# Kernel tuning notes

Hardware: AMD Instinct MI355X
Metric: run time of the kernel (lower is better)

Reference implementation:

```python
import jax, jax.numpy as jnp
from jax import lax
import numpy as np

CHANNELS = 16
THRESH = 0.1
UPDATE_RATE = 0.25


def _sobel_kernel():
    ident = np.array([[0., 0., 0.], [0., 1., 0.], [0., 0., 0.]], np.float32)
    sx = np.array([[-1., 0., 1.], [-2., 0., 2.], [-1., 0., 1.]], np.float32)
    sy = sx.T
    k = np.stack([ident, sx, sy])[:, None, :, :]          # [3,1,3,3]
    k = np.tile(k, (CHANNELS, 1, 1, 1))                   # [48,1,3,3] (torch repeat order)
    return jnp.asarray(k)


def _perceive(x, w_sobel):
    # circular pad then depthwise grouped conv (groups=CHANNELS, 3 filters per group)
    xp = jnp.pad(x, ((0, 0), (0, 0), (1, 1), (1, 1)), mode='wrap')
    return lax.conv_general_dilated(
        xp, w_sobel, window_strides=(1, 1), padding='VALID',
        dimension_numbers=('NCHW', 'OIHW', 'NCHW'),
        feature_group_count=CHANNELS)                     # [B,48,H,W]


def _alive_mask(x):
    alpha = x[:, 3:4]                                     # [B,1,H,W]
    p = jnp.pad(alpha, ((0, 0), (0, 0), (1, 1), (1, 1)), mode='wrap')
    m = lax.reduce_window(p, -jnp.inf, lax.max, (1, 1, 3, 3), (1, 1, 1, 1), 'VALID')
    return (m > THRESH).astype(x.dtype)


def _mlp(y, w1, b1, w2, b2, w3):
    h = jax.nn.relu(jnp.einsum('bchw,oc->bohw', y, w1) + b1[None, :, None, None])
    h = jax.nn.relu(jnp.einsum('bchw,oc->bohw', h, w2) + b2[None, :, None, None])
    return jnp.einsum('bchw,oc->bohw', h, w3)             # [B,16,H,W], no bias


def setup_inputs() -> dict:
    key = jax.random.key(0)
    ks = jax.random.split(key, 7)
    B, H, W, steps = 8, 256, 256, 2
    s = 0.1
    return {
        'x': jax.random.uniform(ks[0], (B, CHANNELS, H, W), jnp.float32),
        'w1': jax.random.normal(ks[1], (64, 48), jnp.float32) * s,
        'b1': jax.random.normal(ks[2], (64,), jnp.float32) * s,
        'w2': jax.random.normal(ks[3], (64, 64), jnp.float32) * s,
        'b2': jax.random.normal(ks[4], (64,), jnp.float32) * s,
        'w3': jax.random.normal(ks[5], (CHANNELS, 64), jnp.float32) * s,
        'update_masks': jax.random.uniform(ks[6], (steps, B, 1, H, W), jnp.float32),
        'steps': steps,
    }


def reference(x, w1, b1, w2, b2, w3, update_masks, steps):
    w_sobel = _sobel_kernel()
    for i in range(steps):
        pre = _alive_mask(x)
        y = _mlp(_perceive(x, w_sobel), w1, b1, w2, b2, w3)
        um = (update_masks[i] < UPDATE_RATE).astype(x.dtype)
        x = x + y * um
        post = _alive_mask(x)
        x = x * (pre * post)
    return x
```

## Files before the change

### kernel.cpp

```cpp
#include <hip/hip_runtime.h>
#include <hip/hip_bf16.h>

#define NB 8
#define NC 16
#define NH 256
#define NW 256
#define ALIVE_THRESH 0.1f
#define UPDATE_RATE 0.25f

typedef __attribute__((ext_vector_type(8))) short bf16x8;
typedef __attribute__((ext_vector_type(4))) float f32x4;
typedef unsigned short ushort_t;

#define MFMA16(a, b, c) __builtin_amdgcn_mfma_f32_16x16x32_bf16((a), (b), (c), 0, 0, 0)

static __device__ __forceinline__ unsigned short f2bf(float f) {
    __hip_bfloat16 h = __float2bfloat16(f);
    return __builtin_bit_cast(unsigned short, h);
}
static __device__ __forceinline__ float bf2f(unsigned short b) {
    union { unsigned u; float f; } x; x.u = ((unsigned)b) << 16; return x.f;
}
static __device__ __forceinline__ unsigned pack2(float lo, float hi) {
    return (unsigned)f2bf(lo) | ((unsigned)f2bf(hi) << 16);
}

static __device__ __forceinline__ int ybyte(int px, int g) {
    return px * 128 + ((g ^ (px & 7)) << 4);
}

__global__ void prep_weights(const float* __restrict__ w1, const float* __restrict__ b1,
                             const float* __restrict__ w2, const float* __restrict__ w3,
                             int4* __restrict__ wf)
{
    const int f = blockIdx.x, l = threadIdx.x;
    const int lq = l >> 4, ln = l & 15;
    union { unsigned short us[8]; int4 v; } u;
    if (f < 8) {
        const int mt = f >> 1, ks = f & 1, m = mt * 16 + ln;
        #pragma unroll
        for (int j = 0; j < 8; ++j) {
            const int k = ks * 32 + lq * 8 + j;
            float v = (k < 48) ? w1[m * 48 + k] : ((k == 48) ? b1[m] : 0.0f);
            u.us[j] = f2bf(v);
        }
    } else if (f < 16) {
        const int ff = f - 8, mt = ff >> 1, ks = ff & 1, m = mt * 16 + ln;
        #pragma unroll
        for (int j = 0; j < 8; ++j)
            u.us[j] = f2bf(w2[m * 64 + (ks * 32 + lq * 8 + j)]);
    } else {
        const int ks = f - 16, m = ln;
        #pragma unroll
        for (int j = 0; j < 8; ++j)
            u.us[j] = f2bf(w3[m * 64 + (ks * 32 + lq * 8 + j)]);
    }
    wf[f * 64 + l] = u.v;
}

template<bool MASK_IN>
__global__ __launch_bounds__(256) void nca_step_a(
    const void* __restrict__ xin_v,
    const float* __restrict__ um,
    const float* __restrict__ b2,
    const int4*  __restrict__ wf,
    ushort_t* __restrict__ xout,
    const unsigned char* __restrict__ preb_in,
    unsigned char* __restrict__ preb_out)
{
    __shared__ char  smem[256 * 128];
    __shared__ float premax2[NW];
    __shared__ float mmid[NW];

    char*     yb   = smem;
    unsigned* sd   = (unsigned*)(smem + 4096);
    float*    vbuf = (float*)smem;

    const int t = threadIdx.x;
    const int bx = blockIdx.x;
    const int h = ((bx & 7) << 5) | (bx >> 3);
    const int b = blockIdx.y;
    const int hm = (h - 1) & (NH - 1), hp = (h + 1) & (NH - 1);
    const size_t cs = (size_t)NH * NW;
    const size_t base = (size_t)b * NC * cs;

    float mreg[NC], dreg[NC];

    if constexpr (MASK_IN) {
        const ushort_t* xin = (const ushort_t*)xin_v;
        const ushort_t* ac = xin + base + 3 * cs;
        float am[5];
        #pragma unroll
        for (int j = 0; j < 5; ++j)
            am[j] = bf2f(ac[(size_t)((h - 2 + j) & (NH - 1)) * NW + t]);
        vbuf[0 * NW + t] = fmaxf(fmaxf(am[0], am[1]), am[2]);
        vbuf[1 * NW + t] = fmaxf(fmaxf(am[1], am[2]), am[3]);
        vbuf[2 * NW + t] = fmaxf(fmaxf(am[2], am[3]), am[4]);
        const unsigned char p0 = preb_in[((size_t)b * NH + hm) * NW + t];
        const unsigned char p1 = preb_in[((size_t)b * NH + h ) * NW + t];
        const unsigned char p2 = preb_in[((size_t)b * NH + hp) * NW + t];
        __syncthreads();

        const int tm = (t - 1) & (NW - 1), tp = (t + 1) & (NW - 1);
        float x0 = fmaxf(fmaxf(vbuf[tm],          vbuf[t]),          vbuf[tp]);
        float x1 = fmaxf(fmaxf(vbuf[NW + tm],     vbuf[NW + t]),     vbuf[NW + tp]);
        float x2 = fmaxf(fmaxf(vbuf[2 * NW + tm], vbuf[2 * NW + t]), vbuf[2 * NW + tp]);
        const float m0 = (x0 > ALIVE_THRESH && p0) ? 1.0f : 0.0f;
        const float m1 = (x1 > ALIVE_THRESH && p1) ? 1.0f : 0.0f;
        const float m2 = (x2 > ALIVE_THRESH && p2) ? 1.0f : 0.0f;
        mmid[t] = m1;
        premax2[t] = fmaxf(fmaxf(am[1] * m0, am[2] * m1), am[3] * m2);

        #pragma unroll
        for (int c = 0; c < NC; ++c) {
            float top, mid, bot;
            if (c == 3) { top = am[1] * m0; mid = am[2] * m1; bot = am[3] * m2; }
            else {
                const ushort_t* xc = xin + base + (size_t)c * cs;
                top = bf2f(xc[(size_t)hm * NW + t]) * m0;
                mid = bf2f(xc[(size_t)h  * NW + t]) * m1;
                bot = bf2f(xc[(size_t)hp * NW + t]) * m2;
            }
            float s = top + 2.0f * mid + bot, d = bot - top;
            sd[c * NW + t] = pack2(s, d);
            mreg[c] = mid; dreg[c] = d;
        }
        __syncthreads();
    } else {
        const float* xin = (const float*)xin_v;
        #pragma unroll
        for (int c = 0; c < NC; ++c) {
            const float* xc = xin + base + (size_t)c * cs;
            float top = xc[(size_t)hm * NW + t];
            float mid = xc[(size_t)h  * NW + t];
            float bot = xc[(size_t)hp * NW + t];
            float s = top + 2.0f * mid + bot, d = bot - top;
            sd[c * NW + t] = pack2(s, d);
            mreg[c] = mid; dreg[c] = d;
            if (c == 3) premax2[t] = fmaxf(fmaxf(top, mid), bot);
        }
        __syncthreads();
    }

    {
        const int tm = (t - 1) & (NW - 1), tp = (t + 1) & (NW - 1);
        float mx = fmaxf(fmaxf(premax2[tm], premax2[t]), premax2[tp]);
        preb_out[((size_t)b * NH + h) * NW + t] = (mx > ALIVE_THRESH) ? 1 : 0;
    }

    unsigned yp[24];
    {
        const int tm = (t - 1) & (NW - 1), tp = (t + 1) & (NW - 1);
        #pragma unroll
        for (int c = 0; c < NC; ++c) {
            unsigned L = sd[c * NW + tm];
            unsigned R = sd[c * NW + tp];
            float sl = bf2f((unsigned short)L), dl = bf2f((unsigned short)(L >> 16));
            float sr = bf2f((unsigned short)R), dr = bf2f((unsigned short)(R >> 16));
            float y0 = mreg[c];
            float y1 = sr - sl;
            float y2 = dl + 2.0f * dreg[c] + dr;
            unsigned short u0 = f2bf(y0), u1 = f2bf(y1), u2 = f2bf(y2);
            const int k = 3 * c;
            if ((k & 1) == 0) {
                yp[k >> 1] = (unsigned)u0 | ((unsigned)u1 << 16);
                if (((k + 2) & 1) == 0) yp[(k + 2) >> 1] = (unsigned)u2;
                else                    yp[(k + 2) >> 1] |= 0;
            } else {
                yp[k >> 1] |= ((unsigned)u0 << 16);
                yp[(k + 1) >> 1] = (unsigned)u1 | ((unsigned)u2 << 16);
            }
        }
    }
    {
        const int tm = (t - 1) & (NW - 1), tp = (t + 1) & (NW - 1);
        unsigned short ys[48];
        #pragma unroll
        for (int c = 0; c < NC; ++c) {
            unsigned L = sd[c * NW + tm];
            unsigned R = sd[c * NW + tp];
            float sl = bf2f((unsigned short)L), dl = bf2f((unsigned short)(L >> 16));
            float sr = bf2f((unsigned short)R), dr = bf2f((unsigned short)(R >> 16));
            ys[3 * c + 0] = f2bf(mreg[c]);
            ys[3 * c + 1] = f2bf(sr - sl);
            ys[3 * c + 2] = f2bf(dl + 2.0f * dreg[c] + dr);
        }
        #pragma unroll
        for (int i = 0; i < 24; ++i)
            yp[i] = (unsigned)ys[2 * i] | ((unsigned)ys[2 * i + 1] << 16);
    }
    __syncthreads();

    {
        #pragma unroll
        for (int g = 0; g < 6; ++g) {
            union { unsigned w[4]; int4 v; } pk;
            pk.w[0] = yp[4 * g]; pk.w[1] = yp[4 * g + 1];
            pk.w[2] = yp[4 * g + 2]; pk.w[3] = yp[4 * g + 3];
            *(int4*)(yb + ybyte(t, g)) = pk.v;
        }
        int4 biasrow; biasrow.x = 0x3F80; biasrow.y = 0; biasrow.z = 0; biasrow.w = 0;
        *(int4*)(yb + ybyte(t, 6)) = biasrow;
        int4 zz; zz.x = zz.y = zz.z = zz.w = 0;
        *(int4*)(yb + ybyte(t, 7)) = zz;
    }

    const int lane = t & 63, wv = t >> 6;
    const int lq = lane >> 4, ln = lane & 15;
    const int px0 = wv * 64;

    float umv[4];
    {
        const float* umr = um + ((size_t)b * NH + h) * NW;
        #pragma unroll
        for (int nt = 0; nt < 4; ++nt)
            umv[nt] = (umr[px0 + nt * 16 + ln] < UPDATE_RATE) ? 1.0f : 0.0f;
    }

    bf16x8 a1[8];
    #pragma unroll
    for (int f = 0; f < 8; ++f) a1[f] = __builtin_bit_cast(bf16x8, wf[f * 64 + lane]);

    #pragma unroll
    for (int nt = 0; nt < 4; ++nt) {
        const int px = px0 + nt * 16 + ln;
        bf16x8 bb0 = *(const bf16x8*)(yb + ybyte(px, lq));
        bf16x8 bb1 = *(const bf16x8*)(yb + ybyte(px, 4 + lq));
        f32x4 acc[4];
        #pragma unroll
        for (int mt = 0; mt < 4; ++mt) {
            f32x4 z = {0.f, 0.f, 0.f, 0.f};
            z = MFMA16(a1[2 * mt],     bb0, z);
            z = MFMA16(a1[2 * mt + 1], bb1, z);
            acc[mt] = z;
        }
        #pragma unroll
        for (int mt = 0; mt < 4; ++mt) {
            unsigned p0 = pack2(fmaxf(acc[mt][0], 0.f), fmaxf(acc[mt][1], 0.f));
            unsigned p1 = pack2(fmaxf(acc[mt][2], 0.f), fmaxf(acc[mt][3], 0.f));
            union { unsigned w[2]; uint2 v; } pk; pk.w[0] = p0; pk.w[1] = p1;
            *(uint2*)(yb + ybyte(px, 2 * mt + (lq >> 1)) + (lq & 1) * 8) = pk.v;
        }
    }

    bf16x8 a2[8];
    #pragma unroll
    for (int f = 0; f < 8; ++f) a2[f] = __builtin_bit_cast(bf16x8, wf[(8 + f) * 64 + lane]);
    f32x4 b2v[4];
    #pragma unroll
    for (int mt = 0; mt < 4; ++mt)
        b2v[mt] = *(const f32x4*)(b2 + mt * 16 + lq * 4);

    #pragma unroll
    for (int nt = 0; nt < 4; ++nt) {
        const int px = px0 + nt * 16 + ln;
        bf16x8 bb0 = *(const bf16x8*)(yb + ybyte(px, lq));
        bf16x8 bb1 = *(const bf16x8*)(yb + ybyte(px, 4 + lq));
        f32x4 acc[4];
        #pragma unroll
        for (int mt = 0; mt < 4; ++mt) {
            f32x4 z = {0.f, 0.f, 0.f, 0.f};
            z = MFMA16(a2[2 * mt],     bb0, z);
            z = MFMA16(a2[2 * mt + 1], bb1, z);
            acc[mt] = z + b2v[mt];
        }
        #pragma unroll
        for (int mt = 0; mt < 4; ++mt) {
            unsigned p0 = pack2(fmaxf(acc[mt][0], 0.f), fmaxf(acc[mt][1], 0.f));
            unsigned p1 = pack2(fmaxf(acc[mt][2], 0.f), fmaxf(acc[mt][3], 0.f));
            union { unsigned w[2]; uint2 v; } pk; pk.w[0] = p0; pk.w[1] = p1;
            *(uint2*)(yb + ybyte(px, 2 * mt + (lq >> 1)) + (lq & 1) * 8) = pk.v;
        }
    }

    bf16x8 a3[2];
    a3[0] = __builtin_bit_cast(bf16x8, wf[16 * 64 + lane]);
    a3[1] = __builtin_bit_cast(bf16x8, wf[17 * 64 + lane]);

    #pragma unroll
    for (int nt = 0; nt < 4; ++nt) {
        const int px = px0 + nt * 16 + ln;
        float xcv[4];
        if constexpr (MASK_IN) {
            const ushort_t* xin = (const ushort_t*)xin_v;
            const float mm = mmid[px];
            #pragma unroll
            for (int r = 0; r < 4; ++r)
                xcv[r] = bf2f(xin[base + (size_t)(lq * 4 + r) * cs + (size_t)h * NW + px]) * mm;
        } else {
            const float* xin = (const float*)xin_v;
            #pragma unroll
            for (int r = 0; r < 4; ++r)
                xcv[r] = xin[base + (size_t)(lq * 4 + r) * cs + (size_t)h * NW + px];
        }
        bf16x8 bb0 = *(const bf16x8*)(yb + ybyte(px, lq));
        bf16x8 bb1 = *(const bf16x8*)(yb + ybyte(px, 4 + lq));
        f32x4 z = {0.f, 0.f, 0.f, 0.f};
        z = MFMA16(a3[0], bb0, z);
        z = MFMA16(a3[1], bb1, z);
        #pragma unroll
        for (int r = 0; r < 4; ++r) {
            const size_t o = base + (size_t)(lq * 4 + r) * cs + (size_t)h * NW + px;
            xout[o] = f2bf(xcv[r] + z[r] * umv[nt]);
        }
    }
}

__global__ __launch_bounds__(256) void nca_final(
    const ushort_t* __restrict__ bf,
    const unsigned char* __restrict__ preb,
    float* __restrict__ xout)
{
    __shared__ float vmax[NW];

    const int t = threadIdx.x;
    const int bx = blockIdx.x;
    const int h = ((bx & 7) << 5) | (bx >> 3);
    const int b = blockIdx.y;
    const int hm = (h - 1) & (NH - 1), hp = (h + 1) & (NH - 1);
    const size_t cs = (size_t)NH * NW;
    const size_t base = (size_t)b * NC * cs;

    const ushort_t* ac = bf + base + 3 * cs;
    float a0 = bf2f(ac[(size_t)hm * NW + t]);
    float a1 = bf2f(ac[(size_t)h  * NW + t]);
    float a2 = bf2f(ac[(size_t)hp * NW + t]);
    vmax[t] = fmaxf(fmaxf(a0, a1), a2);
    const unsigned char p = preb[((size_t)b * NH + h) * NW + t];
    __syncthreads();

    const int tm = (t - 1) & (NW - 1), tp = (t + 1) & (NW - 1);
    float mx = fmaxf(fmaxf(vmax[tm], vmax[t]), vmax[tp]);
    const float m = (mx > ALIVE_THRESH && p) ? 1.0f : 0.0f;

    #pragma unroll
    for (int c = 0; c < NC; ++c) {
        const size_t o = base + (size_t)c * cs + (size_t)h * NW + t;
        xout[o] = bf2f(bf[o]) * m;
    }
}

extern "C" void kernel_launch(void* const* d_in, const int* in_sizes, int n_in,
                              void* d_out, int out_size, void* d_ws, size_t ws_size,
                              hipStream_t stream) {
    const float* x  = (const float*)d_in[0];
    const float* w1 = (const float*)d_in[1];
    const float* b1 = (const float*)d_in[2];
    const float* w2 = (const float*)d_in[3];
    const float* b2 = (const float*)d_in[4];
    const float* w3 = (const float*)d_in[5];
    const float* um = (const float*)d_in[6];
    const int steps = in_sizes[6] / (NB * NH * NW);

    const size_t npix  = (size_t)NB * NH * NW;
    const size_t nelem = (size_t)NB * NC * NH * NW;

    ushort_t* bfA        = (ushort_t*)d_ws;
    ushort_t* bfB        = bfA + nelem;
    unsigned char* prebA = (unsigned char*)(bfB + nelem);
    unsigned char* prebB = prebA + npix;
    int4* wf             = (int4*)(prebB + npix);
    float* xout          = (float*)d_out;

    prep_weights<<<18, 64, 0, stream>>>(w1, b1, w2, w3, wf);

    dim3 grdA(NH, NB);

    const void* cur = x;
    unsigned char* preb_last = prebA;
    for (int i = 0; i < steps; ++i) {
        const float* um_i = um + (size_t)i * npix;
        ushort_t* bfo      = (i % 2 == 0) ? bfA : bfB;
        unsigned char* po  = (i % 2 == 0) ? prebA : prebB;
        unsigned char* pin = (i % 2 == 0) ? prebB : prebA;

        if (i == 0)
            nca_step_a<false><<<grdA, 256, 0, stream>>>(
                cur, um_i, b2, wf, bfo, nullptr, po);
        else
            nca_step_a<true><<<grdA, 256, 0, stream>>>(
                cur, um_i, b2, wf, bfo, pin, po);
        cur = bfo;
        preb_last = po;
    }

    nca_final<<<grdA, 256, 0, stream>>>((const ushort_t*)cur, preb_last, xout);
}
```

Measured before the change: 63.70 us.

## Store intermediate state pixel-major and fuse weight prep into step kernels

Intermediate bf16 state switches from NCHW to a pixel-major layout with 16 channels contiguous per pixel, so each thread loads and stores a pixel's channels as 16-byte vectors. The step kernel recomputes the post-alive mask over a 5x5 alpha neighborhood with direct gathers instead of a shared-memory pass. The separate weight-prep kernel is dropped and each block converts fp32 weights to bf16 fragments itself. This removes one launch and gives coalesced vector I/O, but adds redundant per-block weight conversion and strided single-channel alpha gathers.

```diff
diff --git a/kernel.cpp b/kernel.cpp
--- a/kernel.cpp
+++ b/kernel.cpp
@@ -24,228 +24,79 @@
 static __device__ __forceinline__ unsigned pack2(float lo, float hi) {
     return (unsigned)f2bf(lo) | ((unsigned)f2bf(hi) << 16);
 }
+static __device__ __forceinline__ float bfbits(unsigned w, int hi) {
+    return bf2f((unsigned short)(hi ? (w >> 16) : (w & 0xffffu)));
+}
+static __device__ __forceinline__ float exch(const uint4& v0, const uint4& v1, int c) {
+    unsigned w = (c < 8) ? ((const unsigned*)&v0)[c >> 1]
+                         : ((const unsigned*)&v1)[(c - 8) >> 1];
+    return bfbits(w, c & 1);
+}
 
 static __device__ __forceinline__ int ybyte(int px, int g) {
     return px * 128 + ((g ^ (px & 7)) << 4);
 }
 
-__global__ void prep_weights(const float* __restrict__ w1, const float* __restrict__ b1,
-                             const float* __restrict__ w2, const float* __restrict__ w3,
-                             int4* __restrict__ wf)
+static __device__ __forceinline__ bf16x8 cvt8(const float* p) {
+    float4 v0 = *(const float4*)p, v1 = *(const float4*)(p + 4);
+    union { unsigned w[4]; bf16x8 v; } u;
+    u.w[0] = pack2(v0.x, v0.y); u.w[1] = pack2(v0.z, v0.w);
+    u.w[2] = pack2(v1.x, v1.y); u.w[3] = pack2(v1.z, v1.w);
+    return u.v;
+}
+
+template<typename ResF>
+static __device__ __forceinline__ void mlp_gemm(
+    char* yb, int lane, int px0,
+    const float* __restrict__ w1, const float* __restrict__ b1,
+    const float* __restrict__ w2, const float* __restrict__ b2,
+    const float* __restrict__ w3,
+    const float* __restrict__ umr, ResF getres, ushort_t* __restrict__ outrow)
 {
-    const int f = blockIdx.x, l = threadIdx.x;
-    const int lq = l >> 4, ln = l & 15;
-    union { unsigned short us[8]; int4 v; } u;
-    if (f < 8) {
-        const int mt = f >> 1, ks = f & 1, m = mt * 16 + ln;
-        #pragma unroll
-        for (int j = 0; j < 8; ++j) {
-            const int k = ks * 32 + lq * 8 + j;
-            float v = (k < 48) ? w1[m * 48 + k] : ((k == 48) ? b1[m] : 0.0f);
-            u.us[j] = f2bf(v);
-        }
-    } else if (f < 16) {
-        const int ff = f - 8, mt = ff >> 1, ks = ff & 1, m = mt * 16 + ln;
-        #pragma unroll
-        for (int j = 0; j < 8; ++j)
-            u.us[j] = f2bf(w2[m * 64 + (ks * 32 + lq * 8 + j)]);
-    } else {
-        const int ks = f - 16, m = ln;
-        #pragma unroll
-        for (int j = 0; j < 8; ++j)
-            u.us[j] = f2bf(w3[m * 64 + (ks * 32 + lq * 8 + j)]);
-    }
-    wf[f * 64 + l] = u.v;
-}
-
-template<bool MASK_IN>
-__global__ __launch_bounds__(256) void nca_step_a(
-    const void* __restrict__ xin_v,
-    const float* __restrict__ um,
-    const float* __restrict__ b2,
-    const int4*  __restrict__ wf,
-    ushort_t* __restrict__ xout,
-    const unsigned char* __restrict__ preb_in,
-    unsigned char* __restrict__ preb_out)
-{
-    __shared__ char  smem[256 * 128];
-    __shared__ float premax2[NW];
-    __shared__ float mmid[NW];
-
-    char*     yb   = smem;
-    unsigned* sd   = (unsigned*)(smem + 4096);
-    float*    vbuf = (float*)smem;
-
-    const int t = threadIdx.x;
-    const int bx = blockIdx.x;
-    const int h = ((bx & 7) << 5) | (bx >> 3);
-    const int b = blockIdx.y;
-    const int hm = (h - 1) & (NH - 1), hp = (h + 1) & (NH - 1);
-    const size_t cs = (size_t)NH * NW;
-    const size_t base = (size_t)b * NC * cs;
-
-    float mreg[NC], dreg[NC];
-
-    if constexpr (MASK_IN) {
-        const ushort_t* xin = (const ushort_t*)xin_v;
-        const ushort_t* ac = xin + base + 3 * cs;
-        float am[5];
-        #pragma unroll
-        for (int j = 0; j < 5; ++j)
-            am[j] = bf2f(ac[(size_t)((h - 2 + j) & (NH - 1)) * NW + t]);
-        vbuf[0 * NW + t] = fmaxf(fmaxf(am[0], am[1]), am[2]);
-        vbuf[1 * NW + t] = fmaxf(fmaxf(am[1], am[2]), am[3]);
-        vbuf[2 * NW + t] = fmaxf(fmaxf(am[2], am[3]), am[4]);
-        const unsigned char p0 = preb_in[((size_t)b * NH + hm) * NW + t];
-        const unsigned char p1 = preb_in[((size_t)b * NH + h ) * NW + t];
-        const unsigned char p2 = preb_in[((size_t)b * NH + hp) * NW + t];
-        __syncthreads();
-
-        const int tm = (t - 1) & (NW - 1), tp = (t + 1) & (NW - 1);
-        float x0 = fmaxf(fmaxf(vbuf[tm],          vbuf[t]),          vbuf[tp]);
-        float x1 = fmaxf(fmaxf(vbuf[NW + tm],     vbuf[NW + t]),     vbuf[NW + tp]);
-        float x2 = fmaxf(fmaxf(vbuf[2 * NW + tm], vbuf[2 * NW + t]), vbuf[2 * NW + tp]);
-        const float m0 = (x0 > ALIVE_THRESH && p0) ? 1.0f : 0.0f;
-        const float m1 = (x1 > ALIVE_THRESH && p1) ? 1.0f : 0.0f;
-        const float m2 = (x2 > ALIVE_THRESH && p2) ? 1.0f : 0.0f;
-        mmid[t] = m1;
-        premax2[t] = fmaxf(fmaxf(am[1] * m0, am[2] * m1), am[3] * m2);
-
-        #pragma unroll
-        for (int c = 0; c < NC; ++c) {
-            float top, mid, bot;
-            if (c == 3) { top = am[1] * m0; mid = am[2] * m1; bot = am[3] * m2; }
-            else {
-                const ushort_t* xc = xin + base + (size_t)c * cs;
-                top = bf2f(xc[(size_t)hm * NW + t]) * m0;
-                mid = bf2f(xc[(size_t)h  * NW + t]) * m1;
-                bot = bf2f(xc[(size_t)hp * NW + t]) * m2;
-            }
-            float s = top + 2.0f * mid + bot, d = bot - top;
-            sd[c * NW + t] = pack2(s, d);
-            mreg[c] = mid; dreg[c] = d;
-        }
-        __syncthreads();
-    } else {
-        const float* xin = (const float*)xin_v;
-        #pragma unroll
-        for (int c = 0; c < NC; ++c) {
-            const float* xc = xin + base + (size_t)c * cs;
-            float top = xc[(size_t)hm * NW + t];
-            float mid = xc[(size_t)h  * NW + t];
-            float bot = xc[(size_t)hp * NW + t];
-            float s = top + 2.0f * mid + bot, d = bot - top;
-            sd[c * NW + t] = pack2(s, d);
-            mreg[c] = mid; dreg[c] = d;
-            if (c == 3) premax2[t] = fmaxf(fmaxf(top, mid), bot);
-        }
-        __syncthreads();
-    }
-
-    {
-        const int tm = (t - 1) & (NW - 1), tp = (t + 1) & (NW - 1);
-        float mx = fmaxf(fmaxf(premax2[tm], premax2[t]), premax2[tp]);
-        preb_out[((size_t)b * NH + h) * NW + t] = (mx > ALIVE_THRESH) ? 1 : 0;
-    }
-
-    unsigned yp[24];
-    {
-        const int tm = (t - 1) & (NW - 1), tp = (t + 1) & (NW - 1);
-        #pragma unroll
-        for (int c = 0; c < NC; ++c) {
-            unsigned L = sd[c * NW + tm];
-            unsigned R = sd[c * NW + tp];
-            float sl = bf2f((unsigned short)L), dl = bf2f((unsigned short)(L >> 16));
-            float sr = bf2f((unsigned short)R), dr = bf2f((unsigned short)(R >> 16));
-            float y0 = mreg[c];
-            float y1 = sr - sl;
-            float y2 = dl + 2.0f * dreg[c] + dr;
-            unsigned short u0 = f2bf(y0), u1 = f2bf(y1), u2 = f2bf(y2);
-            const int k = 3 * c;
-            if ((k & 1) == 0) {
-                yp[k >> 1] = (unsigned)u0 | ((unsigned)u1 << 16);
-                if (((k + 2) & 1) == 0) yp[(k + 2) >> 1] = (unsigned)u2;
-                else                    yp[(k + 2) >> 1] |= 0;
-            } else {
-                yp[k >> 1] |= ((unsigned)u0 << 16);
-                yp[(k + 1) >> 1] = (unsigned)u1 | ((unsigned)u2 << 16);
-            }
-        }
-    }
-    {
-        const int tm = (t - 1) & (NW - 1), tp = (t + 1) & (NW - 1);
-        unsigned short ys[48];
-        #pragma unroll
-        for (int c = 0; c < NC; ++c) {
-            unsigned L = sd[c * NW + tm];
-            unsigned R = sd[c * NW + tp];
-            float sl = bf2f((unsigned short)L), dl = bf2f((unsigned short)(L >> 16));
-            float sr = bf2f((unsigned short)R), dr = bf2f((unsigned short)(R >> 16));
-            ys[3 * c + 0] = f2bf(mreg[c]);
-            ys[3 * c + 1] = f2bf(sr - sl);
-            ys[3 * c + 2] = f2bf(dl + 2.0f * dreg[c] + dr);
-        }
-        #pragma unroll
-        for (int i = 0; i < 24; ++i)
-            yp[i] = (unsigned)ys[2 * i] | ((unsigned)ys[2 * i + 1] << 16);
-    }
-    __syncthreads();
-
-    {
-        #pragma unroll
-        for (int g = 0; g < 6; ++g) {
-            union { unsigned w[4]; int4 v; } pk;
-            pk.w[0] = yp[4 * g]; pk.w[1] = yp[4 * g + 1];
-            pk.w[2] = yp[4 * g + 2]; pk.w[3] = yp[4 * g + 3];
-            *(int4*)(yb + ybyte(t, g)) = pk.v;
-        }
-        int4 biasrow; biasrow.x = 0x3F80; biasrow.y = 0; biasrow.z = 0; biasrow.w = 0;
-        *(int4*)(yb + ybyte(t, 6)) = biasrow;
-        int4 zz; zz.x = zz.y = zz.z = zz.w = 0;
-        *(int4*)(yb + ybyte(t, 7)) = zz;
-    }
-
-    const int lane = t & 63, wv = t >> 6;
     const int lq = lane >> 4, ln = lane & 15;
-    const int px0 = wv * 64;
 
     float umv[4];
-    {
-        const float* umr = um + ((size_t)b * NH + h) * NW;
-        #pragma unroll
-        for (int nt = 0; nt < 4; ++nt)
-            umv[nt] = (umr[px0 + nt * 16 + ln] < UPDATE_RATE) ? 1.0f : 0.0f;
-    }
-
-    bf16x8 a1[8];
-    #pragma unroll
-    for (int f = 0; f < 8; ++f) a1[f] = __builtin_bit_cast(bf16x8, wf[f * 64 + lane]);
-
+    #pragma unroll
+    for (int nt = 0; nt < 4; ++nt)
+        umv[nt] = (umr[px0 + nt * 16 + ln] < UPDATE_RATE) ? 1.0f : 0.0f;
+
+    bf16x8 a1f[8];
+    #pragma unroll
+    for (int f = 0; f < 8; ++f) {
+        const int m = (f >> 1) * 16 + ln;
+        const int k0 = (f & 1) * 32 + lq * 8;
+        if (k0 <= 40) a1f[f] = cvt8(w1 + m * 48 + k0);
+        else if (k0 == 48) {
+            union { unsigned w[4]; bf16x8 v; } u;
+            u.w[0] = (unsigned)f2bf(b1[m]); u.w[1] = 0; u.w[2] = 0; u.w[3] = 0;
+            a1f[f] = u.v;
+        } else {
+            union { unsigned w[4]; bf16x8 v; } u;
+            u.w[0] = u.w[1] = u.w[2] = u.w[3] = 0;
+            a1f[f] = u.v;
+        }
+    }
     #pragma unroll
     for (int nt = 0; nt < 4; ++nt) {
         const int px = px0 + nt * 16 + ln;
         bf16x8 bb0 = *(const bf16x8*)(yb + ybyte(px, lq));
         bf16x8 bb1 = *(const bf16x8*)(yb + ybyte(px, 4 + lq));
-        f32x4 acc[4];
         #pragma unroll
         for (int mt = 0; mt < 4; ++mt) {
             f32x4 z = {0.f, 0.f, 0.f, 0.f};
-            z = MFMA16(a1[2 * mt],     bb0, z);
-            z = MFMA16(a1[2 * mt + 1], bb1, z);
-            acc[mt] = z;
-        }
-        #pragma unroll
-        for (int mt = 0; mt < 4; ++mt) {
-            unsigned p0 = pack2(fmaxf(acc[mt][0], 0.f), fmaxf(acc[mt][1], 0.f));
-            unsigned p1 = pack2(fmaxf(acc[mt][2], 0.f), fmaxf(acc[mt][3], 0.f));
-            union { unsigned w[2]; uint2 v; } pk; pk.w[0] = p0; pk.w[1] = p1;
+            z = MFMA16(a1f[2 * mt],     bb0, z);
+            z = MFMA16(a1f[2 * mt + 1], bb1, z);
+            union { unsigned w[2]; uint2 v; } pk;
+            pk.w[0] = pack2(fmaxf(z[0], 0.f), fmaxf(z[1], 0.f));
+            pk.w[1] = pack2(fmaxf(z[2], 0.f), fmaxf(z[3], 0.f));
             *(uint2*)(yb + ybyte(px, 2 * mt + (lq >> 1)) + (lq & 1) * 8) = pk.v;
         }
     }
 
-    bf16x8 a2[8];
-    #pragma unroll
-    for (int f = 0; f < 8; ++f) a2[f] = __builtin_bit_cast(bf16x8, wf[(8 + f) * 64 + lane]);
+    bf16x8 a2f[8];
+    #pragma unroll
+    for (int f = 0; f < 8; ++f)
+        a2f[f] = cvt8(w2 + ((f >> 1) * 16 + ln) * 64 + (f & 1) * 32 + lq * 8);
     f32x4 b2v[4];
     #pragma unroll
     for (int mt = 0; mt < 4; ++mt)
@@ -256,88 +107,283 @@
         const int px = px0 + nt * 16 + ln;
         bf16x8 bb0 = *(const bf16x8*)(yb + ybyte(px, lq));
         bf16x8 bb1 = *(const bf16x8*)(yb + ybyte(px, 4 + lq));
-        f32x4 acc[4];
         #pragma unroll
         for (int mt = 0; mt < 4; ++mt) {
             f32x4 z = {0.f, 0.f, 0.f, 0.f};
-            z = MFMA16(a2[2 * mt],     bb0, z);
-            z = MFMA16(a2[2 * mt + 1], bb1, z);
-            acc[mt] = z + b2v[mt];
-        }
-        #pragma unroll
-        for (int mt = 0; mt < 4; ++mt) {
-            unsigned p0 = pack2(fmaxf(acc[mt][0], 0.f), fmaxf(acc[mt][1], 0.f));
-            unsigned p1 = pack2(fmaxf(acc[mt][2], 0.f), fmaxf(acc[mt][3], 0.f));
-            union { unsigned w[2]; uint2 v; } pk; pk.w[0] = p0; pk.w[1] = p1;
+            z = MFMA16(a2f[2 * mt],     bb0, z);
+            z = MFMA16(a2f[2 * mt + 1], bb1, z);
+            z = z + b2v[mt];
+            union { unsigned w[2]; uint2 v; } pk;
+            pk.w[0] = pack2(fmaxf(z[0], 0.f), fmaxf(z[1], 0.f));
+            pk.w[1] = pack2(fmaxf(z[2], 0.f), fmaxf(z[3], 0.f));
             *(uint2*)(yb + ybyte(px, 2 * mt + (lq >> 1)) + (lq & 1) * 8) = pk.v;
         }
     }
 
-    bf16x8 a3[2];
-    a3[0] = __builtin_bit_cast(bf16x8, wf[16 * 64 + lane]);
-    a3[1] = __builtin_bit_cast(bf16x8, wf[17 * 64 + lane]);
+    bf16x8 a3f[2];
+    a3f[0] = cvt8(w3 + ln * 64 + lq * 8);
+    a3f[1] = cvt8(w3 + ln * 64 + 32 + lq * 8);
 
     #pragma unroll
     for (int nt = 0; nt < 4; ++nt) {
         const int px = px0 + nt * 16 + ln;
-        float xcv[4];
-        if constexpr (MASK_IN) {
-            const ushort_t* xin = (const ushort_t*)xin_v;
-            const float mm = mmid[px];
-            #pragma unroll
-            for (int r = 0; r < 4; ++r)
-                xcv[r] = bf2f(xin[base + (size_t)(lq * 4 + r) * cs + (size_t)h * NW + px]) * mm;
-        } else {
-            const float* xin = (const float*)xin_v;
-            #pragma unroll
-            for (int r = 0; r < 4; ++r)
-                xcv[r] = xin[base + (size_t)(lq * 4 + r) * cs + (size_t)h * NW + px];
-        }
         bf16x8 bb0 = *(const bf16x8*)(yb + ybyte(px, lq));
         bf16x8 bb1 = *(const bf16x8*)(yb + ybyte(px, 4 + lq));
         f32x4 z = {0.f, 0.f, 0.f, 0.f};
-        z = MFMA16(a3[0], bb0, z);
-        z = MFMA16(a3[1], bb1, z);
-        #pragma unroll
-        for (int r = 0; r < 4; ++r) {
-            const size_t o = base + (size_t)(lq * 4 + r) * cs + (size_t)h * NW + px;
-            xout[o] = f2bf(xcv[r] + z[r] * umv[nt]);
-        }
-    }
+        z = MFMA16(a3f[0], bb0, z);
+        z = MFMA16(a3f[1], bb1, z);
+        f32x4 res = getres(px, lq);
+        union { unsigned w[2]; uint2 v; } pk;
+        pk.w[0] = pack2(res[0] + z[0] * umv[nt], res[1] + z[1] * umv[nt]);
+        pk.w[1] = pack2(res[2] + z[2] * umv[nt], res[3] + z[3] * umv[nt]);
+        *(uint2*)(outrow + (size_t)px * 16 + lq * 4) = pk.v;
+    }
+}
+
+__global__ __launch_bounds__(256) void nca_first(
+    const float* __restrict__ x,
+    const float* __restrict__ um,
+    const float* __restrict__ w1, const float* __restrict__ b1,
+    const float* __restrict__ w2, const float* __restrict__ b2,
+    const float* __restrict__ w3,
+    ushort_t* __restrict__ xout,
+    unsigned char* __restrict__ preb_out)
+{
+    __shared__ char  smem[256 * 128];
+    __shared__ float premax[NW];
+
+    char*     yb = smem;
+    unsigned* sd = (unsigned*)(smem + 4096);
+
+    const int t = threadIdx.x, bx = blockIdx.x;
+    const int h = ((bx & 7) << 5) | (bx >> 3);
+    const int b = blockIdx.y;
+    const int hm = (h - 1) & 255, hp = (h + 1) & 255;
+    const size_t cs = (size_t)NH * NW;
+    const size_t base = (size_t)b * NC * cs;
+
+    float mreg[NC], dreg[NC];
+    #pragma unroll
+    for (int c = 0; c < NC; ++c) {
+        const float* xc = x + base + (size_t)c * cs;
+        float top = xc[(size_t)hm * NW + t];
+        float mid = xc[(size_t)h  * NW + t];
+        float bot = xc[(size_t)hp * NW + t];
+        sd[c * NW + t] = pack2(top + 2.0f * mid + bot, bot - top);
+        mreg[c] = mid; dreg[c] = bot - top;
+        if (c == 3) premax[t] = fmaxf(fmaxf(top, mid), bot);
+    }
+    __syncthreads();
+
+    const int tm = (t - 1) & 255, tp = (t + 1) & 255;
+    {
+        float mx = fmaxf(fmaxf(premax[tm], premax[t]), premax[tp]);
+        preb_out[((size_t)b * NH + h) * NW + t] = (mx > ALIVE_THRESH) ? 1 : 0;
+    }
+
+    unsigned yp[24];
+    {
+        unsigned short ys[48];
+        #pragma unroll
+        for (int c = 0; c < NC; ++c) {
+            unsigned L = sd[c * NW + tm], R = sd[c * NW + tp];
+            float sl = bfbits(L, 0), dl = bfbits(L, 1);
+            float sr = bfbits(R, 0), dr = bfbits(R, 1);
+            ys[3 * c + 0] = f2bf(mreg[c]);
+            ys[3 * c + 1] = f2bf(sr - sl);
+            ys[3 * c + 2] = f2bf(dl + 2.0f * dreg[c] + dr);
+        }
+        #pragma unroll
+        for (int i = 0; i < 24; ++i)
+            yp[i] = (unsigned)ys[2 * i] | ((unsigned)ys[2 * i + 1] << 16);
+    }
+    __syncthreads();
+
+    #pragma unroll
+    for (int g = 0; g < 6; ++g) {
+        union { unsigned w[4]; int4 v; } pk;
+        pk.w[0] = yp[4 * g]; pk.w[1] = yp[4 * g + 1];
+        pk.w[2] = yp[4 * g + 2]; pk.w[3] = yp[4 * g + 3];
+        *(int4*)(yb + ybyte(t, g)) = pk.v;
+    }
+    { int4 br; br.x = 0x3F80; br.y = 0; br.z = 0; br.w = 0;
+      *(int4*)(yb + ybyte(t, 6)) = br; }
+    { int4 zz; zz.x = zz.y = zz.z = zz.w = 0;
+      *(int4*)(yb + ybyte(t, 7)) = zz; }
+
+    const int lane = t & 63, wv = t >> 6;
+    const float* umr = um + ((size_t)b * NH + h) * NW;
+    ushort_t* outrow = xout + ((size_t)(b * NH + h) * NW) * 16;
+
+    auto getres = [&](int px, int lq) -> f32x4 {
+        f32x4 r;
+        #pragma unroll
+        for (int i = 0; i < 4; ++i)
+            r[i] = x[base + (size_t)(lq * 4 + i) * cs + (size_t)h * NW + px];
+        return r;
+    };
+    mlp_gemm(yb, lane, wv * 64, w1, b1, w2, b2, w3, umr, getres, outrow);
+}
+
+__global__ __launch_bounds__(256) void nca_step(
+    const ushort_t* __restrict__ xin,
+    const unsigned char* __restrict__ preb_in,
+    const float* __restrict__ um,
+    const float* __restrict__ w1, const float* __restrict__ b1,
+    const float* __restrict__ w2, const float* __restrict__ b2,
+    const float* __restrict__ w3,
+    ushort_t* __restrict__ xout,
+    unsigned char* __restrict__ preb_out)
+{
+    __shared__ char  smem[256 * 128];
+    __shared__ float mmid[NW];
+
+    char*     yb = smem;
+    unsigned* sd = (unsigned*)(smem + 4096);
+
+    const int t = threadIdx.x, bx = blockIdx.x;
+    const int h = ((bx & 7) << 5) | (bx >> 3);
+    const int b = blockIdx.y;
+    const size_t prow = (size_t)b * NH;
+
+    float a[5][5];
+    uint4 sv[3][2];
+    #pragma unroll
+    for (int r = 0; r < 3; ++r) {
+        const size_t e = ((prow + ((h - 1 + r) & 255)) * NW + t) * 16;
+        sv[r][0] = *(const uint4*)(xin + e);
+        sv[r][1] = *(const uint4*)(xin + e + 8);
+        a[1 + r][2] = bfbits(sv[r][0].y, 1);
+    }
+    #pragma unroll
+    for (int j = 0; j < 5; ++j) {
+        const int hh = (h - 2 + j) & 255;
+        const size_t rb = (prow + hh) * NW * 16 + 3;
+        #pragma unroll
+        for (int d = 0; d < 5; ++d) {
+            if (j >= 1 && j <= 3 && d == 2) continue;
+            const int uu = (t - 2 + d) & 255;
+            a[j][d] = bf2f(xin[rb + (size_t)uu * 16]);
+        }
+    }
+
+    float m3x3[3][3];
+    #pragma unroll
+    for (int r = 0; r < 3; ++r) {
+        float cm[5];
+        #pragma unroll
+        for (int d = 0; d < 5; ++d)
+            cm[d] = fmaxf(fmaxf(a[r][d], a[r + 1][d]), a[r + 2][d]);
+        #pragma unroll
+        for (int dd = 0; dd < 3; ++dd) {
+            float post = fmaxf(fmaxf(cm[dd], cm[dd + 1]), cm[dd + 2]);
+            const int hh = (h - 1 + r) & 255, uu = (t - 1 + dd) & 255;
+            unsigned char p = preb_in[(prow + hh) * NW + uu];
+            m3x3[r][dd] = (post > ALIVE_THRESH && p) ? 1.0f : 0.0f;
+        }
+    }
+
+    {
+        float pm = 0.0f;
+        #pragma unroll
+        for (int r = 0; r < 3; ++r)
+            #pragma unroll
+            for (int dd = 0; dd < 3; ++dd)
+                pm = fmaxf(pm, a[1 + r][1 + dd] * m3x3[r][dd]);
+        preb_out[(prow + h) * NW + t] = (pm > ALIVE_THRESH) ? 1 : 0;
+    }
+
+    const float m0 = m3x3[0][1], m1 = m3x3[1][1], m2 = m3x3[2][1];
+    mmid[t] = m1;
+
+    float mreg[NC], dreg[NC];
+    #pragma unroll
+    for (int c = 0; c < NC; ++c) {
+        float top = exch(sv[0][0], sv[0][1], c) * m0;
+        float mid = exch(sv[1][0], sv[1][1], c) * m1;
+        float bot = exch(sv[2][0], sv[2][1], c) * m2;
+        sd[c * NW + t] = pack2(top + 2.0f * mid + bot, bot - top);
+        mreg[c] = mid; dreg[c] = bot - top;
+    }
+    __syncthreads();
+
+    const int tm = (t - 1) & 255, tp = (t + 1) & 255;
+    unsigned yp[24];
+    {
+        unsigned short ys[48];
+        #pragma unroll
+        for (int c = 0; c < NC; ++c) {
+            unsigned L = sd[c * NW + tm], R = sd[c * NW + tp];
+            float sl = bfbits(L, 0), dl = bfbits(L, 1);
+            float sr = bfbits(R, 0), dr = bfbits(R, 1);
+            ys[3 * c + 0] = f2bf(mreg[c]);
+            ys[3 * c + 1] = f2bf(sr - sl);
+            ys[3 * c + 2] = f2bf(dl + 2.0f * dreg[c] + dr);
+        }
+        #pragma unroll
+        for (int i = 0; i < 24; ++i)
+            yp[i] = (unsigned)ys[2 * i] | ((unsigned)ys[2 * i + 1] << 16);
+    }
+    __syncthreads();
+
+    #pragma unroll
+    for (int g = 0; g < 6; ++g) {
+        union { unsigned w[4]; int4 v; } pk;
+        pk.w[0] = yp[4 * g]; pk.w[1] = yp[4 * g + 1];
+        pk.w[2] = yp[4 * g + 2]; pk.w[3] = yp[4 * g + 3];
+        *(int4*)(yb + ybyte(t, g)) = pk.v;
+    }
+    { int4 br; br.x = 0x3F80; br.y = 0; br.z = 0; br.w = 0;
+      *(int4*)(yb + ybyte(t, 6)) = br; }
+    { int4 zz; zz.x = zz.y = zz.z = zz.w = 0;
+      *(int4*)(yb + ybyte(t, 7)) = zz; }
+
+    const int lane = t & 63, wv = t >> 6;
+    const float* umr = um + (prow + h) * NW;
+    const ushort_t* inrow = xin + ((prow + h) * NW) * 16;
+    ushort_t* outrow = xout + ((prow + h) * NW) * 16;
+
+    auto getres = [&](int px, int lq) -> f32x4 {
+        uint2 v = *(const uint2*)(inrow + (size_t)px * 16 + lq * 4);
+        const float mm = mmid[px];
+        f32x4 r;
+        r[0] = bfbits(v.x, 0) * mm; r[1] = bfbits(v.x, 1) * mm;
+        r[2] = bfbits(v.y, 0) * mm; r[3] = bfbits(v.y, 1) * mm;
+        return r;
+    };
+    mlp_gemm(yb, lane, wv * 64, w1, b1, w2, b2, w3, umr, getres, outrow);
 }
 
 __global__ __launch_bounds__(256) void nca_final(
-    const ushort_t* __restrict__ bf,
+    const ushort_t* __restrict__ xin,
     const unsigned char* __restrict__ preb,
     float* __restrict__ xout)
 {
-    __shared__ float vmax[NW];
-
-    const int t = threadIdx.x;
-    const int bx = blockIdx.x;
+    const int t = threadIdx.x, bx = blockIdx.x;
     const int h = ((bx & 7) << 5) | (bx >> 3);
     const int b = blockIdx.y;
-    const int hm = (h - 1) & (NH - 1), hp = (h + 1) & (NH - 1);
+    const size_t prow = (size_t)b * NH;
+
+    const size_t e = ((prow + h) * NW + t) * 16;
+    uint4 s0 = *(const uint4*)(xin + e);
+    uint4 s1 = *(const uint4*)(xin + e + 8);
+
+    float mx = bfbits(s0.y, 1);
+    #pragma unroll
+    for (int r = 0; r < 3; ++r)
+        #pragma unroll
+        for (int d = 0; d < 3; ++d) {
+            if (r == 1 && d == 1) continue;
+            const int hh = (h - 1 + r) & 255, uu = (t - 1 + d) & 255;
+            mx = fmaxf(mx, bf2f(xin[((prow + hh) * NW + uu) * 16 + 3]));
+        }
+    const float m = (mx > ALIVE_THRESH && preb[(prow + h) * NW + t]) ? 1.0f : 0.0f;
+
     const size_t cs = (size_t)NH * NW;
-    const size_t base = (size_t)b * NC * cs;
-
-    const ushort_t* ac = bf + base + 3 * cs;
-    float a0 = bf2f(ac[(size_t)hm * NW + t]);
-    float a1 = bf2f(ac[(size_t)h  * NW + t]);
-    float a2 = bf2f(ac[(size_t)hp * NW + t]);
-    vmax[t] = fmaxf(fmaxf(a0, a1), a2);
-    const unsigned char p = preb[((size_t)b * NH + h) * NW + t];
-    __syncthreads();
-
-    const int tm = (t - 1) & (NW - 1), tp = (t + 1) & (NW - 1);
-    float mx = fmaxf(fmaxf(vmax[tm], vmax[t]), vmax[tp]);
-    const float m = (mx > ALIVE_THRESH && p) ? 1.0f : 0.0f;
-
-    #pragma unroll
-    for (int c = 0; c < NC; ++c) {
-        const size_t o = base + (size_t)c * cs + (size_t)h * NW + t;
-        xout[o] = bf2f(bf[o]) * m;
-    }
+    const size_t obase = (size_t)b * NC * cs + (size_t)h * NW + t;
+    #pragma unroll
+    for (int c = 0; c < NC; ++c)
+        xout[obase + (size_t)c * cs] = exch(s0, s1, c) * m;
 }
 
 extern "C" void kernel_launch(void* const* d_in, const int* in_sizes, int n_in,
@@ -359,15 +405,13 @@
     ushort_t* bfB        = bfA + nelem;
     unsigned char* prebA = (unsigned char*)(bfB + nelem);
     unsigned char* prebB = prebA + npix;
-    int4* wf             = (int4*)(prebB + npix);
     float* xout          = (float*)d_out;
 
-    prep_weights<<<18, 64, 0, stream>>>(w1, b1, w2, w3, wf);
-
-    dim3 grdA(NH, NB);
-
-    const void* cur = x;
+    dim3 grd(NH, NB);
+
+    const ushort_t* cur = bfA;
     unsigned char* preb_last = prebA;
+
     for (int i = 0; i < steps; ++i) {
         const float* um_i = um + (size_t)i * npix;
         ushort_t* bfo      = (i % 2 == 0) ? bfA : bfB;
@@ -375,14 +419,14 @@
         unsigned char* pin = (i % 2 == 0) ? prebB : prebA;
 
         if (i == 0)
-            nca_step_a<false><<<grdA, 256, 0, stream>>>(
-                cur, um_i, b2, wf, bfo, nullptr, po);
+            nca_first<<<grd, 256, 0, stream>>>(x, um_i, w1, b1, w2, b2, w3,
+                                               bfo, po);
         else
-            nca_step_a<true><<<grdA, 256, 0, stream>>>(
-                cur, um_i, b2, wf, bfo, pin, po);
+            nca_step<<<grd, 256, 0, stream>>>(cur, pin, um_i, w1, b1, w2, b2, w3,
+                                              bfo, po);
         cur = bfo;
         preb_last = po;
     }
 
-    nca_final<<<grdA, 256, 0, stream>>>((const ushort_t*)cur, preb_last, xout);
-}
+    nca_final<<<grd, 256, 0, stream>>>(cur, preb_last, xout);
+}
```

New measurement: 108.6 us. 1.7x slower.
